# Kernel optimization log

Measured on AMD Instinct MI355X. Metric: run time of the kernel, lower is better.

## Reference

```python
import jax, jax.numpy as jnp
import numpy as np

B, T, I, H, O = 4096, 512, 1, 64, 1


def setup_inputs() -> dict:
    key = jax.random.key(0)
    ks = jax.random.split(key, 7)
    s = 1.0 / np.sqrt(H)  # PyTorch default init scale
    return {
        "x": jax.random.normal(ks[0], (B, T, I), dtype=jnp.float32),
        "w_ih": jax.random.uniform(ks[1], (4 * H, I), jnp.float32, -s, s),
        "w_hh": jax.random.uniform(ks[2], (4 * H, H), jnp.float32, -s, s),
        "b_ih": jax.random.uniform(ks[3], (4 * H,), jnp.float32, -s, s),
        "b_hh": jax.random.uniform(ks[4], (4 * H,), jnp.float32, -s, s),
        "w_out": jax.random.uniform(ks[5], (O, H), jnp.float32, -s, s),
        "b_out": jax.random.uniform(ks[6], (O,), jnp.float32, -s, s),
    }


def reference(x, w_ih, w_hh, b_ih, b_hh, w_out, b_out):
    # x: [B, T, I]; PyTorch gate order in 4H dim is (i, f, g, o)
    b = b_ih + b_hh  # [4H]
    # precompute input projections for all timesteps: [T, B, 4H]
    xg = jnp.einsum("bti,gi->tbg", x, w_ih) + b

    def step(carry, xg_t):
        h, c = carry  # [B, H] each
        gates = xg_t + h @ w_hh.T  # [B, 4H]
        i, f, g, o = jnp.split(gates, 4, axis=-1)
        i = jax.nn.sigmoid(i)
        f = jax.nn.sigmoid(f)
        g = jnp.tanh(g)
        o = jax.nn.sigmoid(o)
        c = f * c + i * g
        h = o * jnp.tanh(c)
        return (h, c), None

    nb = x.shape[0]
    h0 = jnp.zeros((nb, w_hh.shape[1]), x.dtype)
    (h_T, _), _ = jax.lax.scan(step, (h0, h0), xg)
    # linear on last hidden state only (lstm_out[:, -1, :])
    return h_T @ w_out.T + b_out
```

## Files before the change

### kernel.cpp

```cpp
#include <hip/hip_runtime.h>


#define TT   512
#define MB   8
#define HP   72
#define BUFE (16 * HP)
#define SXP  10

#define L2E  1.4426950408889634f
#define L2E2 2.8853900817779268f

typedef _Float16 f16x8 __attribute__((ext_vector_type(8)));
typedef float    f32x4 __attribute__((ext_vector_type(4)));
typedef float    f32x2 __attribute__((ext_vector_type(2)));

#define MFMA16(a, b, c) __builtin_amdgcn_mfma_f32_16x16x32_f16((a), (b), (c), 0, 0, 0)

__device__ __forceinline__ float rcp_(float x)  { return __builtin_amdgcn_rcpf(x); }
__device__ __forceinline__ float exp2_(float x) { return __builtin_amdgcn_exp2f(x); }

__device__ __forceinline__ f16x8 cvt8s(const float4& u0, const float4& u1, float s) {
    f16x8 r;
    r[0] = (_Float16)(u0.x * s); r[1] = (_Float16)(u0.y * s);
    r[2] = (_Float16)(u0.z * s); r[3] = (_Float16)(u0.w * s);
    r[4] = (_Float16)(u1.x * s); r[5] = (_Float16)(u1.y * s);
    r[6] = (_Float16)(u1.z * s); r[7] = (_Float16)(u1.w * s);
    return r;
}

__global__ __launch_bounds__(256, 2) void lstm_mfma(
    const float* __restrict__ x,
    const float* __restrict__ w_ih,
    const float* __restrict__ w_hh,
    const float* __restrict__ b_ih,
    const float* __restrict__ b_hh,
    const float* __restrict__ w_out,
    const float* __restrict__ b_out,
    float* __restrict__ out)
{
    __shared__ __align__(16) float    sh_x[TT * SXP];
    __shared__ __align__(16) _Float16 hbuf[2 * BUFE];

    const int tid = threadIdx.x;
    const int w   = tid >> 6;
    const int L   = tid & 63;
    const int l16 = L & 15;
    const int h0  = L >> 4;
    const int b0  = blockIdx.x * MB;
    const int j   = 16 * w + l16;

    {
        const int q = tid >> 5;
        const int l = tid & 31;
        const float* xr = x + (size_t)(b0 + q) * TT;
        #pragma unroll
        for (int i = 0; i < TT / 32; ++i)
            sh_x[(l + 32 * i) * SXP + q] = xr[l + 32 * i];
    }
    for (int i = tid; i < 2 * BUFE; i += 256) hbuf[i] = (_Float16)0.0f;

    const float sc[4] = {-L2E, -L2E, L2E2, -L2E};
    f16x8 Bf[4][2];
    float wihv[4], biasv[4];
    #pragma unroll
    for (int s = 0; s < 4; ++s) {
        const int n = 64 * s + j;
        #pragma unroll
        for (int kt = 0; kt < 2; ++kt) {
            const float* p = w_hh + n * 64 + kt * 32 + h0 * 8;
            float4 u0 = *(const float4*)p;
            float4 u1 = *(const float4*)(p + 4);
            Bf[s][kt] = cvt8s(u0, u1, sc[s]);
        }
        wihv[s]  = w_ih[n] * sc[s];
        biasv[s] = (b_ih[n] + b_hh[n]) * sc[s];
    }

    const int aoff = l16 * HP + h0 * 8;
    const int xoff = 2 * h0;
    const int wr   = 4 * h0 * HP + j;

    f32x2 ccv = {0.0f, 0.0f};

    f32x4 ci[4];
    {
        const float2 x0 = *(const float2*)(sh_x + xoff);
        #pragma unroll
        for (int s = 0; s < 4; ++s) {
            ci[s][0] = fmaf(x0.x, wihv[s], biasv[s]);
            ci[s][1] = 0.0f;
            ci[s][2] = fmaf(x0.y, wihv[s], biasv[s]);
            ci[s][3] = 0.0f;
        }
    }

    __syncthreads();

    if (((blockIdx.x >> 8) ^ blockIdx.x) & 1) {
        __builtin_amdgcn_s_sleep(10);
    }

    auto step = [&](const _Float16* rb, _Float16* wb, int t) {
        f16x8 a0 = *(const f16x8*)(rb + aoff);
        f16x8 a1 = *(const f16x8*)(rb + aoff + 32);

        f32x4 acc[4];
        #pragma unroll
        for (int s = 0; s < 4; ++s)
            acc[s] = MFMA16(a1, Bf[s][1], MFMA16(a0, Bf[s][0], ci[s]));

        if (t + 1 < TT) {
            const float2 xn = *(const float2*)(sh_x + (t + 1) * SXP + xoff);
            const f32x2 xnv = {xn.x, xn.y};
            #pragma unroll
            for (int s = 0; s < 4; ++s) {
                f32x2 c2 = xnv * wihv[s] + biasv[s];
                ci[s][0] = c2[0];
                ci[s][2] = c2[1];
            }
        }

        f32x2 Ei = {exp2_(acc[0][0]), exp2_(acc[0][2])};
        f32x2 Ef = {exp2_(acc[1][0]), exp2_(acc[1][2])};
        f32x2 Eg = {exp2_(acc[2][0]), exp2_(acc[2][2])};
        f32x2 Eo = {exp2_(acc[3][0]), exp2_(acc[3][2])};
        f32x2 Di = Ei + 1.0f, Df = Ef + 1.0f, Dg = Eg + 1.0f, Do = Eo + 1.0f;

        f32x2 FG = Df * Dg, IG = Di * Dg, IF = Di * Df;
        f32x2 P  = Di * FG;
        float u  = rcp_(P[0] * P[1]);
        f32x2 inv = {u * P[1], u * P[0]};

        f32x2 si = FG * inv, sf = IG * inv;
        f32x2 tg = 1.0f - 2.0f * (IF * inv);
        ccv = sf * ccv + si * tg;

        f32x2 ca = ccv * L2E2;
        f32x2 Ec = {exp2_(fminf(ca[0], 30.0f)), exp2_(fminf(ca[1], 30.0f))};
        f32x2 Dc = Ec + 1.0f;
        f32x2 Q  = Do * Dc;
        float v  = rcp_(Q[0] * Q[1]);
        f32x2 iq = {v * Q[1], v * Q[0]};
        f32x2 hv = (iq * Dc) * (1.0f - 2.0f * (iq * Do));

        wb[wr]          = (_Float16)hv[0];
        wb[wr + 2 * HP] = (_Float16)hv[1];
        __syncthreads();
    };

    for (int t = 0; t < TT; t += 2) {
        step(hbuf,        hbuf + BUFE, t);
        step(hbuf + BUFE, hbuf,        t + 1);
    }

    const float wo = w_out[L];
    #pragma unroll
    for (int p = 0; p < 2; ++p) {
        const int q = 2 * w + p;
        float v = (float)hbuf[(2 * q) * HP + L] * wo;
        #pragma unroll
        for (int off = 32; off; off >>= 1) v += __shfl_down(v, off);
        if (L == 0) out[b0 + q] = v + b_out[0];
    }
}

extern "C" void kernel_launch(void* const* d_in, const int* in_sizes, int n_in,
                              void* d_out, int out_size, void* d_ws, size_t ws_size,
                              hipStream_t stream) {
    const float* x     = (const float*)d_in[0];
    const float* w_ih  = (const float*)d_in[1];
    const float* w_hh  = (const float*)d_in[2];
    const float* b_ih  = (const float*)d_in[3];
    const float* b_hh  = (const float*)d_in[4];
    const float* w_out = (const float*)d_in[5];
    const float* b_out = (const float*)d_in[6];
    float* out = (float*)d_out;

    lstm_mfma<<<4096 / MB, 256, 0, stream>>>(x, w_ih, w_hh, b_ih, b_hh,
                                             w_out, b_out, out);
}
```

Baseline: 307.0 us.

## Switch to single-wave blocks of four sequences, dropping per-step barriers

Restructures the LSTM recurrence so each 64-thread block (one wavefront) handles four sequences and computes all 16 gate tiles itself, removing the per-timestep __syncthreads and the double-buffered hidden state. The hidden state is written to LDS in a replicated layout so the next step's MFMA A-operand reads land in the right lanes without cross-wave sync. This trades barrier latency for 4x more MFMAs per wave, a much larger register footprint (16x2 B fragments plus 16 accumulators), and only one wave per block, with 1024 blocks instead of 512. It relies on wave-synchronous LDS ordering within a single wavefront, with no explicit barrier between the hidden-state writes and the next step's reads.

New measurement: 432.3 us. +40.8%, slower.

```diff
diff --git a/kernel.cpp b/kernel.cpp
--- a/kernel.cpp
+++ b/kernel.cpp
@@ -1,11 +1,9 @@
 #include <hip/hip_runtime.h>
 
 
-#define TT   512
-#define MB   8
-#define HP   72
-#define BUFE (16 * HP)
-#define SXP  10
+#define TT  512
+#define HP  72
+#define SXQ 4
 
 #define L2E  1.4426950408889634f
 #define L2E2 2.8853900817779268f
@@ -28,7 +26,7 @@
     return r;
 }
 
-__global__ __launch_bounds__(256, 2) void lstm_mfma(
+__global__ __launch_bounds__(64, 1) void lstm_sw(
     const float* __restrict__ x,
     const float* __restrict__ w_ih,
     const float* __restrict__ w_hh,
@@ -38,126 +36,119 @@
     const float* __restrict__ b_out,
     float* __restrict__ out)
 {
-    __shared__ __align__(16) float    sh_x[TT * SXP];
-    __shared__ __align__(16) _Float16 hbuf[2 * BUFE];
+    __shared__ __align__(16) float    sh_x[TT * SXQ];
+    __shared__ __align__(16) _Float16 hb[16 * HP];
 
-    const int tid = threadIdx.x;
-    const int w   = tid >> 6;
-    const int L   = tid & 63;
+    const int L   = threadIdx.x;
     const int l16 = L & 15;
     const int h0  = L >> 4;
-    const int b0  = blockIdx.x * MB;
-    const int j   = 16 * w + l16;
+    const int b0  = blockIdx.x * 4;
 
-    {
-        const int q = tid >> 5;
-        const int l = tid & 31;
+    #pragma unroll
+    for (int q = 0; q < 4; ++q) {
         const float* xr = x + (size_t)(b0 + q) * TT;
         #pragma unroll
-        for (int i = 0; i < TT / 32; ++i)
-            sh_x[(l + 32 * i) * SXP + q] = xr[l + 32 * i];
+        for (int i = 0; i < 2; ++i) {
+            const int t0 = 4 * (L + 64 * i);
+            float4 v = *(const float4*)(xr + t0);
+            sh_x[(t0 + 0) * SXQ + q] = v.x;
+            sh_x[(t0 + 1) * SXQ + q] = v.y;
+            sh_x[(t0 + 2) * SXQ + q] = v.z;
+            sh_x[(t0 + 3) * SXQ + q] = v.w;
+        }
     }
-    for (int i = tid; i < 2 * BUFE; i += 256) hbuf[i] = (_Float16)0.0f;
+    #pragma unroll
+    for (int i = L; i < 16 * HP; i += 64) hb[i] = (_Float16)0.0f;
 
     const float sc[4] = {-L2E, -L2E, L2E2, -L2E};
-    f16x8 Bf[4][2];
-    float wihv[4], biasv[4];
+    f16x8 Bf[16][2];
+    float wihv[16], biasv[16];
     #pragma unroll
-    for (int s = 0; s < 4; ++s) {
-        const int n = 64 * s + j;
+    for (int p = 0; p < 16; ++p) {
+        const int n = 16 * p + l16;
+        const float s = sc[p >> 2];
         #pragma unroll
-        for (int kt = 0; kt < 2; ++kt) {
-            const float* p = w_hh + n * 64 + kt * 32 + h0 * 8;
-            float4 u0 = *(const float4*)p;
-            float4 u1 = *(const float4*)(p + 4);
-            Bf[s][kt] = cvt8s(u0, u1, sc[s]);
+        for (int c = 0; c < 2; ++c) {
+            const float* w0 = w_hh + n * 64 + 32 * c + 8 * h0;
+            float4 u0 = *(const float4*)w0;
+            float4 u1 = *(const float4*)(w0 + 4);
+            Bf[p][c] = cvt8s(u0, u1, s);
         }
-        wihv[s]  = w_ih[n] * sc[s];
-        biasv[s] = (b_ih[n] + b_hh[n]) * sc[s];
+        wihv[p]  = w_ih[n] * s;
+        biasv[p] = (b_ih[n] + b_hh[n]) * s;
     }
 
-    const int aoff = l16 * HP + h0 * 8;
-    const int xoff = 2 * h0;
-    const int wr   = 4 * h0 * HP + j;
+    const int  qb   = 2 * (h0 & 1);
+    const bool hi   = (h0 >> 1) != 0;
+    const int  aoff = l16 * HP + 8 * h0;
+    const int  uc   = (hi ? 32 : 0) + l16;
+    const int  wr0  = (2 * qb) * HP;
+    const int  wr1  = (2 * qb + 2) * HP;
 
-    f32x2 ccv = {0.0f, 0.0f};
+    f32x2 cca = {0.0f, 0.0f};
+    f32x2 ccb = {0.0f, 0.0f};
 
-    f32x4 ci[4];
-    {
-        const float2 x0 = *(const float2*)(sh_x + xoff);
-        #pragma unroll
-        for (int s = 0; s < 4; ++s) {
-            ci[s][0] = fmaf(x0.x, wihv[s], biasv[s]);
-            ci[s][1] = 0.0f;
-            ci[s][2] = fmaf(x0.y, wihv[s], biasv[s]);
-            ci[s][3] = 0.0f;
-        }
-    }
-
-    __syncthreads();
-
-    if (((blockIdx.x >> 8) ^ blockIdx.x) & 1) {
-        __builtin_amdgcn_s_sleep(10);
-    }
-
-    auto step = [&](const _Float16* rb, _Float16* wb, int t) {
-        f16x8 a0 = *(const f16x8*)(rb + aoff);
-        f16x8 a1 = *(const f16x8*)(rb + aoff + 32);
-
-        f32x4 acc[4];
-        #pragma unroll
-        for (int s = 0; s < 4; ++s)
-            acc[s] = MFMA16(a1, Bf[s][1], MFMA16(a0, Bf[s][0], ci[s]));
-
-        if (t + 1 < TT) {
-            const float2 xn = *(const float2*)(sh_x + (t + 1) * SXP + xoff);
-            const f32x2 xnv = {xn.x, xn.y};
-            #pragma unroll
-            for (int s = 0; s < 4; ++s) {
-                f32x2 c2 = xnv * wihv[s] + biasv[s];
-                ci[s][0] = c2[0];
-                ci[s][2] = c2[1];
-            }
-        }
-
-        f32x2 Ei = {exp2_(acc[0][0]), exp2_(acc[0][2])};
-        f32x2 Ef = {exp2_(acc[1][0]), exp2_(acc[1][2])};
-        f32x2 Eg = {exp2_(acc[2][0]), exp2_(acc[2][2])};
-        f32x2 Eo = {exp2_(acc[3][0]), exp2_(acc[3][2])};
+    auto pair_up = [&](f32x2 ai, f32x2 af, f32x2 ag, f32x2 ao, f32x2& cc) -> f32x2 {
+        f32x2 Ei = {exp2_(ai[0]), exp2_(ai[1])};
+        f32x2 Ef = {exp2_(af[0]), exp2_(af[1])};
+        f32x2 Eg = {exp2_(ag[0]), exp2_(ag[1])};
+        f32x2 Eo = {exp2_(ao[0]), exp2_(ao[1])};
         f32x2 Di = Ei + 1.0f, Df = Ef + 1.0f, Dg = Eg + 1.0f, Do = Eo + 1.0f;
-
         f32x2 FG = Df * Dg, IG = Di * Dg, IF = Di * Df;
         f32x2 P  = Di * FG;
         float u  = rcp_(P[0] * P[1]);
         f32x2 inv = {u * P[1], u * P[0]};
-
         f32x2 si = FG * inv, sf = IG * inv;
         f32x2 tg = 1.0f - 2.0f * (IF * inv);
-        ccv = sf * ccv + si * tg;
-
-        f32x2 ca = ccv * L2E2;
+        cc = sf * cc + si * tg;
+        f32x2 ca = cc * L2E2;
         f32x2 Ec = {exp2_(fminf(ca[0], 30.0f)), exp2_(fminf(ca[1], 30.0f))};
         f32x2 Dc = Ec + 1.0f;
         f32x2 Q  = Do * Dc;
         float v  = rcp_(Q[0] * Q[1]);
         f32x2 iq = {v * Q[1], v * Q[0]};
-        f32x2 hv = (iq * Dc) * (1.0f - 2.0f * (iq * Do));
-
-        wb[wr]          = (_Float16)hv[0];
-        wb[wr + 2 * HP] = (_Float16)hv[1];
-        __syncthreads();
+        return (iq * Dc) * (1.0f - 2.0f * (iq * Do));
     };
 
-    for (int t = 0; t < TT; t += 2) {
-        step(hbuf,        hbuf + BUFE, t);
-        step(hbuf + BUFE, hbuf,        t + 1);
+    for (int t = 0; t < TT; ++t) {
+        f16x8 A0 = *(const f16x8*)(hb + aoff);
+        f16x8 A1 = *(const f16x8*)(hb + aoff + 32);
+        const float2 xv = *(const float2*)(sh_x + SXQ * t + qb);
+        const float cx0 = xv.x, cx1 = xv.y;
+
+        f32x4 acc[16];
+        #pragma unroll
+        for (int p = 0; p < 16; ++p) {
+            f32x4 c0 = {fmaf(cx0, wihv[p], biasv[p]), 0.0f,
+                        fmaf(cx1, wihv[p], biasv[p]), 0.0f};
+            acc[p] = MFMA16(A1, Bf[p][1], MFMA16(A0, Bf[p][0], c0));
+        }
+
+        #define GS(tau, e) (hi ? (f32x2){acc[4*(tau)+2][e], acc[4*(tau)+3][e]} \
+                               : (f32x2){acc[4*(tau)+0][e], acc[4*(tau)+1][e]})
+        f32x2 Ai0 = GS(0, 0), Af0 = GS(1, 0), Ag0 = GS(2, 0), Ao0 = GS(3, 0);
+        f32x2 Ai1 = GS(0, 2), Af1 = GS(1, 2), Ag1 = GS(2, 2), Ao1 = GS(3, 2);
+        #undef GS
+
+        f32x2 hva = pair_up(Ai0, Af0, Ag0, Ao0, cca);
+        f32x2 hvb = pair_up(Ai1, Af1, Ag1, Ao1, ccb);
+
+        _Float16 a0 = (_Float16)hva[0], a1 = (_Float16)hva[1];
+        _Float16 b0h = (_Float16)hvb[0], b1h = (_Float16)hvb[1];
+        hb[wr0 + uc]               = a0;
+        hb[wr0 + uc + 16]          = a1;
+        hb[wr0 + 8 * HP + uc]      = a0;
+        hb[wr0 + 8 * HP + uc + 16] = a1;
+        hb[wr1 + uc]               = b0h;
+        hb[wr1 + uc + 16]          = b1h;
+        hb[wr1 + 8 * HP + uc]      = b0h;
+        hb[wr1 + 8 * HP + uc + 16] = b1h;
     }
 
     const float wo = w_out[L];
     #pragma unroll
-    for (int p = 0; p < 2; ++p) {
-        const int q = 2 * w + p;
-        float v = (float)hbuf[(2 * q) * HP + L] * wo;
+    for (int q = 0; q < 4; ++q) {
+        float v = (float)hb[(2 * q) * HP + L] * wo;
         #pragma unroll
         for (int off = 32; off; off >>= 1) v += __shfl_down(v, off);
         if (L == 0) out[b0 + q] = v + b_out[0];
@@ -176,6 +167,6 @@
     const float* b_out = (const float*)d_in[6];
     float* out = (float*)d_out;
 
-    lstm_mfma<<<4096 / MB, 256, 0, stream>>>(x, w_ih, w_hh, b_ih, b_hh,
-                                             w_out, b_out, out);
+    lstm_sw<<<1024, 64, 0, stream>>>(x, w_ih, w_hh, b_ih, b_hh,
+                                     w_out, b_out, out);
 }
```
